# Kernel optimization log

Measured on AMD Instinct MI355X. Metric: run time of the kernel, lower is better.

Reference implementation:

```python
import jax, jax.numpy as jnp
import numpy as np

NEG = -9.0e9  # the -9000000000.0 sentinel used by the torch code


def _masked_bidir_scores(first, second, fmask, smask):
    """Vectorized form of the BxB python double loop in score_grounding.
    first: (B,N,D), second: (B,L,D), fmask: (B,N), smask: (B,L).
    Returns sent_scores (B,B) and mention_scores (B,N,L) (= diagonal att)."""
    mask = fmask[:, None, :, None] * smask[None, :, None, :]          # (B,B,N,L)
    avg = jnp.where(mask != 0, mask, NEG)
    am_first = jax.nn.softmax(avg, axis=2)                            # softmax over N (dim=0 per pair)
    am_second = jax.nn.softmax(avg, axis=3)                           # softmax over L (dim=1 per pair)
    dot = jnp.einsum('ind,jld->ijnl', first, second)                  # (B,B,N,L)
    attm = dot * mask
    att = jnp.where(attm * mask != 0, attm, NEG)
    aw_first = jax.nn.softmax(att, axis=3) * mask                     # softmax(att, dim=-1)*mask
    aw_second = jnp.transpose(
        jax.nn.softmax(jnp.swapaxes(att, 2, 3), axis=3) * jnp.swapaxes(mask, 2, 3), (0, 1, 3, 2)
    )                                                                 # softmax(att.T,-1)*mask.T, transposed back
    sent = (jnp.sum(aw_first * att * am_first, axis=(2, 3))
            + jnp.sum(aw_second * att * am_second, axis=(2, 3)))      # (B,B)
    B = first.shape[0]
    mention = att[jnp.arange(B), jnp.arange(B)]                       # diagonal pairs (B,N,L)
    return sent, mention


def _pairwise_mlp(first, second, W1, b1, W2, b2, W3, b3):
    # SimplePairWiseClassifier: MLP over cat(first, second, first*second); dropout=0 (eval-deterministic)
    x = jnp.concatenate([first, second, first * second], axis=-1)     # (..., 3D)
    h = jax.nn.relu(x @ W1 + b1)
    h = jax.nn.relu(h @ W2 + b2)
    return (h @ W3 + b3)[..., 0]


def setup_inputs() -> dict:
    key = jax.random.key(0)
    ks = jax.random.split(key, 12)
    B, Nt, Ns, L, D, H = 32, 64, 48, 36, 1024, 1024

    def mask(k, n):
        m = (jax.random.uniform(k, (B, n)) < 0.85).astype(jnp.float32)
        return m.at[:, :2].set(1.0)  # guarantee no all-zero rows

    return {
        'text_embeddings': jax.random.normal(ks[0], (B, Nt, D), jnp.float32),
        'span_embeddings': jax.random.normal(ks[1], (B, Ns, D), jnp.float32),
        'image_embeddings': jax.random.normal(ks[2], (B, L, D), jnp.float32),
        'text_mask': mask(ks[3], Nt),
        'span_mask': mask(ks[4], Ns),
        'image_mask': mask(ks[5], L),
        'W1': jax.random.normal(ks[6], (3 * D, H), jnp.float32) * 0.02,
        'b1': jnp.zeros((H,), jnp.float32),
        'W2': jax.random.normal(ks[7], (H, H), jnp.float32) * 0.02,
        'b2': jnp.zeros((H,), jnp.float32),
        'W3': jax.random.normal(ks[8], (H, 1), jnp.float32) * 0.02,
        'b3': jnp.zeros((1,), jnp.float32),
    }


def reference(text_embeddings, span_embeddings, image_embeddings,
              text_mask, span_mask, image_mask, W1, b1, W2, b2, W3, b3):
    B, Ns, D = span_embeddings.shape
    # calculate_loss
    S, _ = _masked_bidir_scores(text_embeddings, image_embeddings, text_mask, image_mask)
    # span_emb.view(B, N, -1, D).mean(dim=2) is identity for (B,Ns,D)
    _, grounding_scores = _masked_bidir_scores(span_embeddings, image_embeddings, span_mask, image_mask)
    # score_text over all span pairs (itertools.combinations order == triu_indices k=1)
    fi, si = np.triu_indices(Ns, k=1)
    text_scores = _pairwise_mlp(span_embeddings[:, fi], span_embeddings[:, si],
                                W1, b1, W2, b2, W3, b3)               # (B, Ns*(Ns-1)/2)
    # contrastive retrieval loss over the BxB sentence-image score matrix
    loss = -(jnp.trace(jax.nn.log_softmax(S, axis=1))
             + jnp.trace(jax.nn.log_softmax(S.T, axis=1))) / B
    return loss, grounding_scores, text_scores
```

## Files before the change

### kernel.cpp

```cpp
#include <hip/hip_runtime.h>
#include <math.h>
#include <stdint.h>

#define B_    32
#define NT    64
#define NS    48
#define LI    36
#define D_    1024
#define H_    1024
#define NPAIR 1128
#define ROWS  (B_*NPAIR)
#define NEGV  -9.0e9f
#define NROWT 282
#define CPX   36

typedef _Float16 half8 __attribute__((ext_vector_type(8)));
typedef float floatx4 __attribute__((ext_vector_type(4)));
typedef __attribute__((address_space(3))) uint32_t lds_u32;
typedef __attribute__((address_space(1))) const uint32_t glb_u32;

#define GLOAD16(src, dst) __builtin_amdgcn_global_load_lds((glb_u32*)(src), (lds_u32*)(dst), 16, 0, 0)


template<int EPI, int REMAP>
__global__ __launch_bounds__(256) void mfma_gemm(
    const _Float16* __restrict__ A, const _Float16* __restrict__ Bt,
    float* __restrict__ Cf, float* __restrict__ scores,
    const float* __restrict__ bias, const float* __restrict__ W3,
    int N, int K) {
  __shared__ __align__(16) _Float16 sA[8192];
  __shared__ __align__(16) _Float16 sB[8192];
  __shared__ float sRed[128][2];
  int rowT, colT;
  if (REMAP) {
    int bid = blockIdx.x;
    int x = bid & 7, ord = bid >> 3;
    rowT = x * CPX + (ord >> 3);
    colT = ord & 7;
    if (rowT >= NROWT) return;
  } else {
    rowT = blockIdx.y; colT = blockIdx.x;
  }
  const int rowBase = rowT * 128, colBase = colT * 128;
  const int tid = threadIdx.x;
  const int lane = tid & 63;
  const int wave = tid >> 6;
  const int wr = wave >> 1, wc = wave & 1;
  const int l15 = lane & 15, l16 = lane >> 4;
  const int rsw = (l15 >> 1) & 3;

  const int sRow = tid >> 2;
  const int swz8 = (((tid & 3) ^ ((tid >> 3) & 3)) << 3);
  const _Float16* gA = A + (size_t)(rowBase + sRow) * K + swz8;
  const _Float16* gB = Bt + (size_t)(colBase + sRow) * K + swz8;
  _Float16* lA = sA + tid * 8;
  _Float16* lB = sB + tid * 8;

  floatx4 acc[4][4] = {};
  for (int k0 = 0; k0 < K; k0 += 64) {
    GLOAD16(gA + k0,               lA);
    GLOAD16(gA + 64 * K + k0,      lA + 2048);
    GLOAD16(gA + k0 + 32,          lA + 4096);
    GLOAD16(gA + 64 * K + k0 + 32, lA + 6144);
    GLOAD16(gB + k0,               lB);
    GLOAD16(gB + 64 * K + k0,      lB + 2048);
    GLOAD16(gB + k0 + 32,          lB + 4096);
    GLOAD16(gB + 64 * K + k0 + 32, lB + 6144);
    __syncthreads();
#pragma unroll
    for (int h = 0; h < 2; ++h) {
      const int hb = h * 4096;
      half8 aF[4], bF[4];
#pragma unroll
      for (int i = 0; i < 4; ++i)
        aF[i] = *(const half8*)&sA[hb + (wr * 64 + i * 16 + l15) * 32 + ((l16 ^ rsw) << 3)];
#pragma unroll
      for (int j = 0; j < 4; ++j)
        bF[j] = *(const half8*)&sB[hb + (wc * 64 + j * 16 + l15) * 32 + ((l16 ^ rsw) << 3)];
#pragma unroll
      for (int i = 0; i < 4; ++i)
#pragma unroll
        for (int j = 0; j < 4; ++j)
          acc[i][j] = __builtin_amdgcn_mfma_f32_16x16x32_f16(aF[i], bF[j], acc[i][j], 0, 0, 0);
    }
    __syncthreads();
  }

  if (EPI == 0) {
#pragma unroll
    for (int i = 0; i < 4; ++i)
#pragma unroll
      for (int q = 0; q < 4; ++q) {
        int r = rowBase + wr * 64 + i * 16 + l16 * 4 + q;
#pragma unroll
        for (int j = 0; j < 4; ++j) {
          int c = colBase + wc * 64 + j * 16 + l15;
          Cf[(size_t)r * N + c] = acc[i][j][q];
        }
      }
  } else {
    float bv[4], wv[4];
#pragma unroll
    for (int j = 0; j < 4; ++j) {
      int c = colBase + wc * 64 + j * 16 + l15;
      bv[j] = bias[c];
      wv[j] = W3[c];
    }
#pragma unroll
    for (int i = 0; i < 4; ++i)
#pragma unroll
      for (int q = 0; q < 4; ++q) {
        float s = 0.f;
#pragma unroll
        for (int j = 0; j < 4; ++j) s += fmaxf(acc[i][j][q] + bv[j], 0.f) * wv[j];
        s += __shfl_xor(s, 1); s += __shfl_xor(s, 2);
        s += __shfl_xor(s, 4); s += __shfl_xor(s, 8);
        if (l15 == 0) sRed[wr * 64 + i * 16 + l16 * 4 + q][wc] = s;
      }
    __syncthreads();
    if (tid < 128)
      atomicAdd(&scores[rowBase + tid], sRed[tid][0] + sRed[tid][1]);
  }
}

__global__ __launch_bounds__(256) void gemm1_fused(
    const _Float16* __restrict__ spanH, const _Float16* __restrict__ W1cT,
    const float* __restrict__ AB1, const float* __restrict__ b1,
    _Float16* __restrict__ h1out,
    const int* __restrict__ idxF, const int* __restrict__ idxS) {
  __shared__ __align__(16) _Float16 sF[8192];
  __shared__ __align__(16) _Float16 sS[8192];
  __shared__ __align__(16) _Float16 sB[8192];
  __shared__ int sIF[128], sIS[128];
  int bid = blockIdx.x;
  int x = bid & 7, ord = bid >> 3;
  int rowT = x * CPX + (ord >> 3);
  int colT = ord & 7;
  if (rowT >= NROWT) return;
  const int rowBase = rowT * 128, colBase = colT * 128;
  const int tid = threadIdx.x;
  const int lane = tid & 63;
  const int wave = tid >> 6;
  const int wr = wave >> 1, wc = wave & 1;
  const int l15 = lane & 15, l16 = lane >> 4;
  const int rsw = (l15 >> 1) & 3;

  if (tid < 128) {
    int rg = rowBase + tid;
    sIF[tid] = idxF[rg];
    sIS[tid] = idxS[rg];
  }
  __syncthreads();

  const int sRow = tid >> 2;
  const int swz8 = (((tid & 3) ^ ((tid >> 3) & 3)) << 3);
  const _Float16* gF0 = spanH + (size_t)sIF[sRow] * D_ + swz8;
  const _Float16* gF1 = spanH + (size_t)sIF[sRow + 64] * D_ + swz8;
  const _Float16* gS0 = spanH + (size_t)sIS[sRow] * D_ + swz8;
  const _Float16* gS1 = spanH + (size_t)sIS[sRow + 64] * D_ + swz8;
  const _Float16* gB  = W1cT + (size_t)(colBase + sRow) * D_ + swz8;
  _Float16* lF = sF + tid * 8;
  _Float16* lS = sS + tid * 8;
  _Float16* lB = sB + tid * 8;

  floatx4 acc[4][4] = {};
  for (int k0 = 0; k0 < D_; k0 += 64) {
    GLOAD16(gF0 + k0,      lF);
    GLOAD16(gF1 + k0,      lF + 2048);
    GLOAD16(gF0 + k0 + 32, lF + 4096);
    GLOAD16(gF1 + k0 + 32, lF + 6144);
    GLOAD16(gS0 + k0,      lS);
    GLOAD16(gS1 + k0,      lS + 2048);
    GLOAD16(gS0 + k0 + 32, lS + 4096);
    GLOAD16(gS1 + k0 + 32, lS + 6144);
    GLOAD16(gB + k0,               lB);
    GLOAD16(gB + 64 * D_ + k0,     lB + 2048);
    GLOAD16(gB + k0 + 32,          lB + 4096);
    GLOAD16(gB + 64 * D_ + k0 + 32,lB + 6144);
    __syncthreads();
#pragma unroll
    for (int h = 0; h < 2; ++h) {
      const int hb = h * 4096;
      half8 aF[4], bF[4];
#pragma unroll
      for (int i = 0; i < 4; ++i) {
        int off = hb + (wr * 64 + i * 16 + l15) * 32 + ((l16 ^ rsw) << 3);
        half8 f = *(const half8*)&sF[off];
        half8 s = *(const half8*)&sS[off];
        aF[i] = f * s;
      }
#pragma unroll
      for (int j = 0; j < 4; ++j)
        bF[j] = *(const half8*)&sB[hb + (wc * 64 + j * 16 + l15) * 32 + ((l16 ^ rsw) << 3)];
#pragma unroll
      for (int i = 0; i < 4; ++i)
#pragma unroll
        for (int j = 0; j < 4; ++j)
          acc[i][j] = __builtin_amdgcn_mfma_f32_16x16x32_f16(aF[i], bF[j], acc[i][j], 0, 0, 0);
    }
    __syncthreads();
  }

  int cols[4]; float bv[4];
#pragma unroll
  for (int j = 0; j < 4; ++j) {
    cols[j] = colBase + wc * 64 + j * 16 + l15;
    bv[j] = b1[cols[j]];
  }
#pragma unroll
  for (int i = 0; i < 4; ++i)
#pragma unroll
    for (int q = 0; q < 4; ++q) {
      int rL = wr * 64 + i * 16 + l16 * 4 + q;
      int rG = rowBase + rL;
      const float* ap = AB1 + (size_t)sIF[rL] * 2048;
      const float* bp = AB1 + (size_t)sIS[rL] * 2048 + 1024;
#pragma unroll
      for (int j = 0; j < 4; ++j) {
        int c = cols[j];
        float v = acc[i][j][q] + ap[c] + bp[c] + bv[j];
        h1out[(size_t)rG * 1024 + c] = (_Float16)fmaxf(v, 0.f);
      }
    }
}

__global__ __launch_bounds__(256) void cvt_f16(
    const float* __restrict__ in, _Float16* __restrict__ out, long long n8) {
  long long i = (long long)blockIdx.x * 256 + threadIdx.x;
  if (i >= n8) return;
  const float4* p = (const float4*)in + i * 2;
  float4 a = p[0], b = p[1];
  half8 h;
  h[0] = (_Float16)a.x; h[1] = (_Float16)a.y; h[2] = (_Float16)a.z; h[3] = (_Float16)a.w;
  h[4] = (_Float16)b.x; h[5] = (_Float16)b.y; h[6] = (_Float16)b.z; h[7] = (_Float16)b.w;
  *(half8*)(out + i * 8) = h;
}

__global__ __launch_bounds__(256) void transpose_cvt(
    const float* __restrict__ in, _Float16* __restrict__ out) {
  __shared__ float t[32][33];
  const int tx = threadIdx.x & 31, ty = threadIdx.x >> 5;
  const int k0 = blockIdx.y * 32, n0 = blockIdx.x * 32;
#pragma unroll
  for (int q = 0; q < 4; ++q)
    t[ty + q * 8][tx] = in[(size_t)(k0 + ty + q * 8) * 1024 + n0 + tx];
  __syncthreads();
#pragma unroll
  for (int q = 0; q < 4; ++q)
    out[(size_t)(n0 + ty + q * 8) * 1024 + k0 + tx] = (_Float16)t[tx][ty + q * 8];
}

__global__ __launch_bounds__(256) void idx_init(int* __restrict__ idxF, int* __restrict__ idxS) {
  int r = blockIdx.x * 256 + threadIdx.x;
  if (r >= ROWS) return;
  int bb = r / NPAIR, p = r - bb * NPAIR;
  int cum = 0, f = 0;
  while (true) { int cnt = NS - 1 - f; if (p < cum + cnt) break; cum += cnt; ++f; }
  idxF[r] = bb * NS + f;
  idxS[r] = bb * NS + f + 1 + (p - cum);
}

__global__ void init_scores(float* __restrict__ scores, const float* __restrict__ b3) {
  int idx = blockIdx.x * 256 + threadIdx.x;
  if (idx < ROWS) scores[idx] = b3[0];
}

__global__ __launch_bounds__(256) void extract_grounding(
    const float* __restrict__ dotSI, const float* __restrict__ smask,
    const float* __restrict__ imask, float* __restrict__ outg) {
  int idx = blockIdx.x * 256 + threadIdx.x;
  if (idx >= B_ * NS * LI) return;
  int b = idx / (NS * LI);
  int rem = idx - b * (NS * LI);
  int n = rem / LI, l = rem - n * LI;
  float v = dotSI[(size_t)(b * NS + n) * (B_ * LI) + b * LI + l];
  outg[idx] = (smask[b * NS + n] * imask[b * LI + l] != 0.f) ? v : NEGV;
}

__global__ __launch_bounds__(64) void sent_kernel(
    const float* __restrict__ dotTI, const float* __restrict__ tmask,
    const float* __restrict__ imask, float* __restrict__ S) {
  const int i = blockIdx.y, j = blockIdx.x, t = threadIdx.x;
  __shared__ float red1[64], red2[64];
  const int stride = B_ * LI;
  float e1 = 0.f;
  {
    float tm = tmask[i * NT + t];
    if (tm != 0.f) {
      const float* row = dotTI + (size_t)(i * NT + t) * stride + j * LI;
      float m = -INFINITY;
      for (int l = 0; l < LI; ++l) if (imask[j * LI + l] != 0.f) m = fmaxf(m, row[l]);
      float z = 0.f, w = 0.f;
      for (int l = 0; l < LI; ++l) if (imask[j * LI + l] != 0.f) {
        float d = row[l], p = expf(d - m);
        z += p; w += p * d;
      }
      e1 = w / z;
    }
  }
  red1[t] = e1;
  float e2 = 0.f;
  if (t < LI) {
    float im = imask[j * LI + t];
    if (im != 0.f) {
      const float* col = dotTI + (size_t)(i * NT) * stride + j * LI + t;
      float m = -INFINITY;
      for (int n = 0; n < NT; ++n) if (tmask[i * NT + n] != 0.f) m = fmaxf(m, col[(size_t)n * stride]);
      float z = 0.f, w = 0.f;
      for (int n = 0; n < NT; ++n) if (tmask[i * NT + n] != 0.f) {
        float d = col[(size_t)n * stride], p = expf(d - m);
        z += p; w += p * d;
      }
      e2 = w / z;
    }
  }
  red2[t] = e2;
  __syncthreads();
  if (t == 0) {
    float s1 = 0.f, s2 = 0.f, cn = 0.f, cl = 0.f;
    for (int n = 0; n < NT; ++n) { s1 += red1[n]; cn += tmask[i * NT + n]; }
    for (int l = 0; l < LI; ++l) { s2 += red2[l]; cl += imask[j * LI + l]; }
    S[i * B_ + j] = s1 / cn + s2 / cl;
  }
}

__global__ __launch_bounds__(64) void loss_kernel(
    const float* __restrict__ S, float* __restrict__ out) {
  __shared__ float sS[B_][B_ + 1];
  __shared__ float acc[B_];
  const int t = threadIdx.x;
  for (int e = t; e < B_ * B_; e += 64) sS[e / B_][e % B_] = S[e];
  __syncthreads();
  if (t < B_) {
    float m = -INFINITY;
    for (int j = 0; j < B_; ++j) m = fmaxf(m, sS[t][j]);
    float z = 0.f;
    for (int j = 0; j < B_; ++j) z += expf(sS[t][j] - m);
    float lr = m + logf(z);
    float m2 = -INFINITY;
    for (int i = 0; i < B_; ++i) m2 = fmaxf(m2, sS[i][t]);
    float z2 = 0.f;
    for (int i = 0; i < B_; ++i) z2 += expf(sS[i][t] - m2);
    float lc = m2 + logf(z2);
    acc[t] = 2.f * sS[t][t] - lr - lc;
  }
  __syncthreads();
  if (t == 0) {
    float s = 0.f;
    for (int i = 0; i < B_; ++i) s += acc[i];
    out[0] = -s / (float)B_;
  }
}

extern "C" void kernel_launch(void* const* d_in, const int* in_sizes, int n_in,
                              void* d_out, int out_size, void* d_ws, size_t ws_size,
                              hipStream_t stream) {
  const float* text  = (const float*)d_in[0];
  const float* span  = (const float*)d_in[1];
  const float* img   = (const float*)d_in[2];
  const float* tmask = (const float*)d_in[3];
  const float* smask = (const float*)d_in[4];
  const float* imask = (const float*)d_in[5];
  const float* W1    = (const float*)d_in[6];
  const float* b1    = (const float*)d_in[7];
  const float* W2    = (const float*)d_in[8];
  const float* b2    = (const float*)d_in[9];
  const float* W3    = (const float*)d_in[10];
  const float* b3    = (const float*)d_in[11];

  float* out     = (float*)d_out;
  float* outLoss = out;
  float* outG    = out + 1;
  float* outT    = out + 1 + (size_t)B_ * NS * LI;

  char* w = (char*)d_ws;
  float*    dotTI = (float*)w;            w += (size_t)(B_*NT) * (B_*LI) * 4;
  float*    dotSI = (float*)w;            w += (size_t)(B_*NS) * (B_*LI) * 4;
  float*    S     = (float*)w;            w += 1024 * 4;
  float*    AB1   = (float*)w;            w += (size_t)1536 * 2048 * 4;
  _Float16* h1    = (_Float16*)w;         w += (size_t)ROWS * 1024 * 2;
  _Float16* textH = (_Float16*)w;         w += (size_t)2048 * 1024 * 2;
  _Float16* spanH = (_Float16*)w;         w += (size_t)1536 * 1024 * 2;
  _Float16* imgH  = (_Float16*)w;         w += (size_t)1152 * 1024 * 2;
  _Float16* W1abT = (_Float16*)w;         w += (size_t)2048 * 1024 * 2;
  _Float16* W1cT  = (_Float16*)w;         w += (size_t)1024 * 1024 * 2;
  _Float16* W2T   = (_Float16*)w;         w += (size_t)1024 * 1024 * 2;
  int*      idxF  = (int*)w;              w += ROWS * 4;
  int*      idxS  = (int*)w;              w += ROWS * 4;
  (void)ws_size; (void)in_sizes; (void)n_in; (void)out_size;

  cvt_f16<<<(2048 * 128 + 255) / 256, 256, 0, stream>>>(text, textH, 2048LL * 128);
  cvt_f16<<<(1536 * 128 + 255) / 256, 256, 0, stream>>>(span, spanH, 1536LL * 128);
  cvt_f16<<<(1152 * 128 + 255) / 256, 256, 0, stream>>>(img, imgH, 1152LL * 128);
  transpose_cvt<<<dim3(32, 32), 256, 0, stream>>>(W1, W1abT);
  transpose_cvt<<<dim3(32, 32), 256, 0, stream>>>(W1 + 1024 * 1024, W1abT + 1024 * 1024);
  transpose_cvt<<<dim3(32, 32), 256, 0, stream>>>(W1 + 2048 * 1024, W1cT);
  transpose_cvt<<<dim3(32, 32), 256, 0, stream>>>(W2, W2T);
  idx_init<<<(ROWS + 255) / 256, 256, 0, stream>>>(idxF, idxS);

  mfma_gemm<0, 0><<<dim3((B_*LI) / 128, (B_*NT) / 128), 256, 0, stream>>>(
      textH, imgH, dotTI, nullptr, nullptr, nullptr, B_ * LI, D_);
  sent_kernel<<<dim3(B_, B_), 64, 0, stream>>>(dotTI, tmask, imask, S);
  loss_kernel<<<1, 64, 0, stream>>>(S, outLoss);

  mfma_gemm<0, 0><<<dim3((B_*LI) / 128, (B_*NS) / 128), 256, 0, stream>>>(
      spanH, imgH, dotSI, nullptr, nullptr, nullptr, B_ * LI, D_);
  extract_grounding<<<(B_*NS*LI + 255) / 256, 256, 0, stream>>>(dotSI, smask, imask, outG);

  mfma_gemm<0, 0><<<dim3(2048 / 128, 1536 / 128), 256, 0, stream>>>(
      spanH, W1abT, AB1, nullptr, nullptr, nullptr, 2048, D_);

  gemm1_fused<<<8 * CPX * 8, 256, 0, stream>>>(
      spanH, W1cT, AB1, b1, h1, idxF, idxS);

  init_scores<<<(ROWS + 255) / 256, 256, 0, stream>>>(outT, b3);
  mfma_gemm<2, 1><<<8 * CPX * 8, 256, 0, stream>>>(
      h1, W2T, nullptr, outT, b2, W3, 1024, H_);
}
```

Baseline: 354.1 us.

## Add 256x256 phased-pipeline GEMM2 and merge small GEMMs and conversion launches

Replaces the second MLP GEMM with a 512-thread, 256x256-tile kernel that double-buffers LDS and interleaves global-to-LDS prefetch with four MFMA quadrant phases. It uses barriers and setprio to keep the matrix units busy. The three independent small GEMMs are merged into one launch, and the conversion and transpose kernels are each merged into one launch, to cut launch overhead and fill the GPU better. The cost is higher register and LDS pressure (128 KB of LDS per block) and hand-tuned waitcnt logic, which is fragile.

```diff
diff --git a/kernel.cpp b/kernel.cpp
--- a/kernel.cpp
+++ b/kernel.cpp
@@ -21,34 +21,171 @@
 
 #define GLOAD16(src, dst) __builtin_amdgcn_global_load_lds((glb_u32*)(src), (lds_u32*)(dst), 16, 0, 0)
 
-
-template<int EPI, int REMAP>
-__global__ __launch_bounds__(256) void mfma_gemm(
+#define MMQ(QR, QC)                                                            \
+  {                                                                            \
+    _Pragma("unroll") for (int i = 0; i < 4; ++i) {                            \
+      _Pragma("unroll") for (int j = 0; j < 2; ++j) {                          \
+        acc[QR * 4 + i][QC * 2 + j] = __builtin_amdgcn_mfma_f32_16x16x32_f16(  \
+            aF[i][0], bF[j][0], acc[QR * 4 + i][QC * 2 + j], 0, 0, 0);         \
+        acc[QR * 4 + i][QC * 2 + j] = __builtin_amdgcn_mfma_f32_16x16x32_f16(  \
+            aF[i][1], bF[j][1], acc[QR * 4 + i][QC * 2 + j], 0, 0, 0);         \
+      }                                                                        \
+    }                                                                          \
+  }
+
+__global__ __launch_bounds__(512, 2) void gemm2_8ph(
+    const _Float16* __restrict__ Am, const _Float16* __restrict__ Bt,
+    float* __restrict__ scores, const float* __restrict__ bias,
+    const float* __restrict__ W3) {
+  __shared__ __align__(16) _Float16 sP[65536];
+  __shared__ float sRed[256][4];
+
+  const int orig = blockIdx.x;
+  const int xcd = orig & 7, pos = orig >> 3;
+  const int wg = (xcd < 4 ? xcd * 71 : 284 + (xcd - 4) * 70) + pos;
+  const int rowBase = (wg >> 2) * 256;
+  const int colBase = (wg & 3) * 256;
+
+  const int t = threadIdx.x;
+  const int wave = t >> 6, lane = t & 63;
+  const int wq_r = wave >> 2, wq_c = wave & 3;
+  const int l15 = lane & 15, l16 = lane >> 4;
+  const int sxor = l15 & 7;
+
+  const int srow0 = t >> 3, srow1 = (512 + t) >> 3;
+  const int lcol0 = ((t & 7) ^ (srow0 & 7)) << 3;
+  const int lcol1 = (((512 + t) & 7) ^ (srow1 & 7)) << 3;
+  const _Float16* aS0 = Am + (size_t)(rowBase + srow0) * D_ + lcol0;
+  const _Float16* aS1 = Am + (size_t)(rowBase + srow1) * D_ + lcol1;
+  const _Float16* bS0 = Bt + (size_t)(colBase + srow0) * D_ + lcol0;
+  const _Float16* bS1 = Bt + (size_t)(colBase + srow1) * D_ + lcol1;
+
+  auto stgA = [&](int kt, int h) {
+    const int db = kt & 1;
+    const size_t so = (size_t)kt * 64 + (size_t)h * 128 * D_;
+    _Float16* d = sP + ((db << 1) + h) * 8192;
+    GLOAD16(aS0 + so, d + t * 8);
+    GLOAD16(aS1 + so, d + 4096 + t * 8);
+  };
+  auto stgB = [&](int kt, int h) {
+    const int db = kt & 1;
+    const size_t so = (size_t)kt * 64 + (size_t)h * 128 * D_;
+    _Float16* d = sP + 32768 + ((db << 1) + h) * 8192;
+    GLOAD16(bS0 + so, d + t * 8);
+    GLOAD16(bS1 + so, d + 4096 + t * 8);
+  };
+
+  const int aRdRow = (wq_r * 64 + l15) * 64;
+  const int bRdRow = (wq_c * 32 + l15) * 64;
+  const int rdSlot0 = ((l16) ^ sxor) << 3;
+  const int rdSlot1 = ((4 + l16) ^ sxor) << 3;
+
+  half8 aF[4][2], bF[2][2];
+  floatx4 acc[8][4] = {};
+
+  auto ldA = [&](int db, int qr) {
+    const _Float16* p = sP + ((db << 1) + qr) * 8192 + aRdRow;
+#pragma unroll
+    for (int i = 0; i < 4; ++i) {
+      aF[i][0] = *(const half8*)(p + i * 1024 + rdSlot0);
+      aF[i][1] = *(const half8*)(p + i * 1024 + rdSlot1);
+    }
+  };
+  auto ldB = [&](int db, int qc) {
+    const _Float16* p = sP + 32768 + ((db << 1) + qc) * 8192 + bRdRow;
+#pragma unroll
+    for (int j = 0; j < 2; ++j) {
+      bF[j][0] = *(const half8*)(p + j * 1024 + rdSlot0);
+      bF[j][1] = *(const half8*)(p + j * 1024 + rdSlot1);
+    }
+  };
+
+  stgB(0, 0); stgA(0, 1); stgA(0, 0); stgB(0, 1); stgB(1, 0); stgA(1, 1);
+  asm volatile("s_waitcnt vmcnt(4)" ::: "memory");
+  __builtin_amdgcn_s_barrier();
+
+#pragma unroll 1
+  for (int kt = 0; kt < 16; ++kt) {
+    const int db = kt & 1;
+    const int kn1 = (kt + 1) & 15, kn2 = (kt + 2) & 15;
+    ldA(db, 0); ldB(db, 0);
+    stgA(kn1, 0);
+    __builtin_amdgcn_sched_barrier(0);
+    __builtin_amdgcn_s_barrier();
+    __builtin_amdgcn_s_setprio(1);
+    MMQ(0, 0);
+    __builtin_amdgcn_s_setprio(0);
+    __builtin_amdgcn_s_barrier();
+    ldA(db, 1);
+    stgB(kn1, 1);
+    __builtin_amdgcn_sched_barrier(0);
+    __builtin_amdgcn_s_barrier();
+    __builtin_amdgcn_s_setprio(1);
+    MMQ(1, 0);
+    __builtin_amdgcn_s_setprio(0);
+    __builtin_amdgcn_s_barrier();
+    ldB(db, 1);
+    stgB(kn2, 0);
+    __builtin_amdgcn_sched_barrier(0);
+    __builtin_amdgcn_s_barrier();
+    __builtin_amdgcn_s_setprio(1);
+    MMQ(1, 1);
+    __builtin_amdgcn_s_setprio(0);
+    __builtin_amdgcn_s_barrier();
+    ldA(db, 0);
+    stgA(kn2, 1);
+    __builtin_amdgcn_sched_barrier(0);
+    asm volatile("s_waitcnt vmcnt(4)" ::: "memory");
+    __builtin_amdgcn_s_barrier();
+    __builtin_amdgcn_s_setprio(1);
+    MMQ(0, 1);
+    __builtin_amdgcn_s_setprio(0);
+    __builtin_amdgcn_s_barrier();
+  }
+
+  float bv[2][2], wv[2][2];
+#pragma unroll
+  for (int qc = 0; qc < 2; ++qc)
+#pragma unroll
+    for (int j = 0; j < 2; ++j) {
+      int c = colBase + qc * 128 + wq_c * 32 + j * 16 + l15;
+      bv[qc][j] = bias[c];
+      wv[qc][j] = W3[c];
+    }
+#pragma unroll
+  for (int qr = 0; qr < 2; ++qr)
+#pragma unroll
+    for (int i = 0; i < 4; ++i)
+#pragma unroll
+      for (int q = 0; q < 4; ++q) {
+        float s = 0.f;
+#pragma unroll
+        for (int qc = 0; qc < 2; ++qc)
+#pragma unroll
+          for (int j = 0; j < 2; ++j)
+            s += fmaxf(acc[qr * 4 + i][qc * 2 + j][q] + bv[qc][j], 0.f) * wv[qc][j];
+        s += __shfl_xor(s, 1); s += __shfl_xor(s, 2);
+        s += __shfl_xor(s, 4); s += __shfl_xor(s, 8);
+        if (l15 == 0)
+          sRed[qr * 128 + wq_r * 64 + i * 16 + l16 * 4 + q][wq_c] = s;
+      }
+  __syncthreads();
+  if (t < 256)
+    atomicAdd(&scores[rowBase + t],
+              sRed[t][0] + sRed[t][1] + sRed[t][2] + sRed[t][3]);
+}
+
+__device__ __forceinline__ void gemm_body(
     const _Float16* __restrict__ A, const _Float16* __restrict__ Bt,
-    float* __restrict__ Cf, float* __restrict__ scores,
-    const float* __restrict__ bias, const float* __restrict__ W3,
-    int N, int K) {
+    float* __restrict__ Cf, int N, int K, int rowBase, int colBase) {
   __shared__ __align__(16) _Float16 sA[8192];
   __shared__ __align__(16) _Float16 sB[8192];
-  __shared__ float sRed[128][2];
-  int rowT, colT;
-  if (REMAP) {
-    int bid = blockIdx.x;
-    int x = bid & 7, ord = bid >> 3;
-    rowT = x * CPX + (ord >> 3);
-    colT = ord & 7;
-    if (rowT >= NROWT) return;
-  } else {
-    rowT = blockIdx.y; colT = blockIdx.x;
-  }
-  const int rowBase = rowT * 128, colBase = colT * 128;
   const int tid = threadIdx.x;
   const int lane = tid & 63;
   const int wave = tid >> 6;
   const int wr = wave >> 1, wc = wave & 1;
   const int l15 = lane & 15, l16 = lane >> 4;
   const int rsw = (l15 >> 1) & 3;
-
   const int sRow = tid >> 2;
   const int swz8 = (((tid & 3) ^ ((tid >> 3) & 3)) << 3);
   const _Float16* gA = A + (size_t)(rowBase + sRow) * K + swz8;
@@ -85,42 +222,27 @@
     }
     __syncthreads();
   }
-
-  if (EPI == 0) {
-#pragma unroll
-    for (int i = 0; i < 4; ++i)
-#pragma unroll
-      for (int q = 0; q < 4; ++q) {
-        int r = rowBase + wr * 64 + i * 16 + l16 * 4 + q;
-#pragma unroll
-        for (int j = 0; j < 4; ++j) {
-          int c = colBase + wc * 64 + j * 16 + l15;
-          Cf[(size_t)r * N + c] = acc[i][j][q];
-        }
+#pragma unroll
+  for (int i = 0; i < 4; ++i)
+#pragma unroll
+    for (int q = 0; q < 4; ++q) {
+      int r = rowBase + wr * 64 + i * 16 + l16 * 4 + q;
+#pragma unroll
+      for (int j = 0; j < 4; ++j) {
+        int c = colBase + wc * 64 + j * 16 + l15;
+        Cf[(size_t)r * N + c] = acc[i][j][q];
       }
-  } else {
-    float bv[4], wv[4];
-#pragma unroll
-    for (int j = 0; j < 4; ++j) {
-      int c = colBase + wc * 64 + j * 16 + l15;
-      bv[j] = bias[c];
-      wv[j] = W3[c];
-    }
-#pragma unroll
-    for (int i = 0; i < 4; ++i)
-#pragma unroll
-      for (int q = 0; q < 4; ++q) {
-        float s = 0.f;
-#pragma unroll
-        for (int j = 0; j < 4; ++j) s += fmaxf(acc[i][j][q] + bv[j], 0.f) * wv[j];
-        s += __shfl_xor(s, 1); s += __shfl_xor(s, 2);
-        s += __shfl_xor(s, 4); s += __shfl_xor(s, 8);
-        if (l15 == 0) sRed[wr * 64 + i * 16 + l16 * 4 + q][wc] = s;
-      }
-    __syncthreads();
-    if (tid < 128)
-      atomicAdd(&scores[rowBase + tid], sRed[tid][0] + sRed[tid][1]);
-  }
+    }
+}
+
+__global__ __launch_bounds__(256) void gemm_trio(
+    const _Float16* __restrict__ textH, const _Float16* __restrict__ imgH,
+    const _Float16* __restrict__ spanH, const _Float16* __restrict__ W1abT,
+    float* __restrict__ dotTI, float* __restrict__ dotSI, float* __restrict__ AB1) {
+  int bid = blockIdx.x;
+  if (bid < 144)      gemm_body(textH, imgH, dotTI, 1152, D_, (bid / 9) * 128, (bid % 9) * 128);
+  else if (bid < 252) { int b = bid - 144; gemm_body(spanH, imgH, dotSI, 1152, D_, (b / 9) * 128, (b % 9) * 128); }
+  else                { int b = bid - 252; gemm_body(spanH, W1abT, AB1, 2048, D_, (b / 16) * 128, (b % 16) * 128); }
 }
 
 __global__ __launch_bounds__(256) void gemm1_fused(
@@ -224,30 +346,45 @@
     }
 }
 
-__global__ __launch_bounds__(256) void cvt_f16(
-    const float* __restrict__ in, _Float16* __restrict__ out, long long n8) {
+__global__ __launch_bounds__(256) void cvt_all(
+    const float* __restrict__ text, const float* __restrict__ span,
+    const float* __restrict__ img, _Float16* __restrict__ textH,
+    _Float16* __restrict__ spanH, _Float16* __restrict__ imgH) {
   long long i = (long long)blockIdx.x * 256 + threadIdx.x;
-  if (i >= n8) return;
-  const float4* p = (const float4*)in + i * 2;
+  const float* src; _Float16* dst; long long off;
+  if (i < 262144)      { src = text; dst = textH; off = i; }
+  else if (i < 458752) { src = span; dst = spanH; off = i - 262144; }
+  else if (i < 606208) { src = img;  dst = imgH;  off = i - 458752; }
+  else return;
+  const float4* p = (const float4*)src + off * 2;
   float4 a = p[0], b = p[1];
   half8 h;
   h[0] = (_Float16)a.x; h[1] = (_Float16)a.y; h[2] = (_Float16)a.z; h[3] = (_Float16)a.w;
   h[4] = (_Float16)b.x; h[5] = (_Float16)b.y; h[6] = (_Float16)b.z; h[7] = (_Float16)b.w;
-  *(half8*)(out + i * 8) = h;
-}
-
-__global__ __launch_bounds__(256) void transpose_cvt(
-    const float* __restrict__ in, _Float16* __restrict__ out) {
-  __shared__ float t[32][33];
+  *(half8*)(dst + off * 8) = h;
+}
+
+__global__ __launch_bounds__(256) void transpose_all(
+    const float* __restrict__ W1, const float* __restrict__ W2,
+    _Float16* __restrict__ W1abT, _Float16* __restrict__ W1cT,
+    _Float16* __restrict__ W2T) {
+  __shared__ float tbuf[32][33];
+  const float* in; _Float16* out;
+  switch (blockIdx.z) {
+    case 0: in = W1;                 out = W1abT;                 break;
+    case 1: in = W1 + 1024 * 1024;   out = W1abT + 1024 * 1024;   break;
+    case 2: in = W1 + 2048 * 1024;   out = W1cT;                  break;
+    default: in = W2;                out = W2T;                   break;
+  }
   const int tx = threadIdx.x & 31, ty = threadIdx.x >> 5;
   const int k0 = blockIdx.y * 32, n0 = blockIdx.x * 32;
 #pragma unroll
   for (int q = 0; q < 4; ++q)
-    t[ty + q * 8][tx] = in[(size_t)(k0 + ty + q * 8) * 1024 + n0 + tx];
+    tbuf[ty + q * 8][tx] = in[(size_t)(k0 + ty + q * 8) * 1024 + n0 + tx];
   __syncthreads();
 #pragma unroll
   for (int q = 0; q < 4; ++q)
-    out[(size_t)(n0 + ty + q * 8) * 1024 + k0 + tx] = (_Float16)t[tx][ty + q * 8];
+    out[(size_t)(n0 + ty + q * 8) * 1024 + k0 + tx] = (_Float16)tbuf[tx][ty + q * 8];
 }
 
 __global__ __launch_bounds__(256) void idx_init(int* __restrict__ idxF, int* __restrict__ idxS) {
@@ -389,31 +526,16 @@
   int*      idxS  = (int*)w;              w += ROWS * 4;
   (void)ws_size; (void)in_sizes; (void)n_in; (void)out_size;
 
-  cvt_f16<<<(2048 * 128 + 255) / 256, 256, 0, stream>>>(text, textH, 2048LL * 128);
-  cvt_f16<<<(1536 * 128 + 255) / 256, 256, 0, stream>>>(span, spanH, 1536LL * 128);
-  cvt_f16<<<(1152 * 128 + 255) / 256, 256, 0, stream>>>(img, imgH, 1152LL * 128);
-  transpose_cvt<<<dim3(32, 32), 256, 0, stream>>>(W1, W1abT);
-  transpose_cvt<<<dim3(32, 32), 256, 0, stream>>>(W1 + 1024 * 1024, W1abT + 1024 * 1024);
-  transpose_cvt<<<dim3(32, 32), 256, 0, stream>>>(W1 + 2048 * 1024, W1cT);
-  transpose_cvt<<<dim3(32, 32), 256, 0, stream>>>(W2, W2T);
+  cvt_all<<<(606208 + 255) / 256, 256, 0, stream>>>(text, span, img, textH, spanH, imgH);
+  transpose_all<<<dim3(32, 32, 4), 256, 0, stream>>>(W1, W2, W1abT, W1cT, W2T);
   idx_init<<<(ROWS + 255) / 256, 256, 0, stream>>>(idxF, idxS);
 
-  mfma_gemm<0, 0><<<dim3((B_*LI) / 128, (B_*NT) / 128), 256, 0, stream>>>(
-      textH, imgH, dotTI, nullptr, nullptr, nullptr, B_ * LI, D_);
+  gemm_trio<<<444, 256, 0, stream>>>(textH, imgH, spanH, W1abT, dotTI, dotSI, AB1);
   sent_kernel<<<dim3(B_, B_), 64, 0, stream>>>(dotTI, tmask, imask, S);
   loss_kernel<<<1, 64, 0, stream>>>(S, outLoss);
-
-  mfma_gemm<0, 0><<<dim3((B_*LI) / 128, (B_*NS) / 128), 256, 0, stream>>>(
-      spanH, imgH, dotSI, nullptr, nullptr, nullptr, B_ * LI, D_);
   extract_grounding<<<(B_*NS*LI + 255) / 256, 256, 0, stream>>>(dotSI, smask, imask, outG);
 
-  mfma_gemm<0, 0><<<dim3(2048 / 128, 1536 / 128), 256, 0, stream>>>(
-      spanH, W1abT, AB1, nullptr, nullptr, nullptr, 2048, D_);
-
-  gemm1_fused<<<8 * CPX * 8, 256, 0, stream>>>(
-      spanH, W1cT, AB1, b1, h1, idxF, idxS);
-
+  gemm1_fused<<<8 * CPX * 8, 256, 0, stream>>>(spanH, W1cT, AB1, b1, h1, idxF, idxS);
   init_scores<<<(ROWS + 255) / 256, 256, 0, stream>>>(outT, b3);
-  mfma_gemm<2, 1><<<8 * CPX * 8, 256, 0, stream>>>(
-      h1, W2T, nullptr, outT, b2, W3, 1024, H_);
-}
+  gemm2_8ph<<<564, 512, 0, stream>>>(h1, W2T, outT, b2, W3);
+}
```

Result: faster. 331.1 us (-6.5%).
